# Performance work log

Hardware: AMD Instinct MI355X
Metric: run time of the kernel (lower is better)

## Reference

```python
import jax, jax.numpy as jnp
import numpy as np

B, S, HID = 1, 4096, 2048
H, KVH, D = 8, 4, 256
QR, KR, VR = 6, 2, 2
WINDOW = 1024
SOFTCAP = 50.0
SCALING = 256.0 ** -0.5  # query_pre_attn_scalar ** -0.5
EPS = 1e-6
NEG = -2.3819763e38


def _rope(x, cos, sin):
    # x: [B,S,R,D]; cos/sin: [S,D//2] -> rotate interleaved complex pairs
    xr = x.reshape(*x.shape[:-1], D // 2, 2)
    x1, x2 = xr[..., 0], xr[..., 1]
    c = cos[None, :, None, :]
    s = sin[None, :, None, :]
    out = jnp.stack([x1 * c - x2 * s, x1 * s + x2 * c], axis=-1)
    return out.reshape(x.shape)


def _rmsnorm(x, w):
    var = jnp.mean(x * x, axis=-1, keepdims=True)
    return x * jax.lax.rsqrt(var + EPS) * (1.0 + w)


def setup_inputs() -> dict:
    key = jax.random.key(0)
    ks = jax.random.split(key, 12)
    sc = HID ** -0.5
    pos = np.arange(S, dtype=np.float32)
    inv = 1.0 / (10000.0 ** (np.arange(0, D, 2, dtype=np.float32) / D))
    fr = pos[:, None] * inv[None, :]
    return {
        'hidden_states': jax.random.normal(ks[0], (B, S, HID), jnp.float32),
        'freqs_cos': jnp.asarray(np.cos(fr), jnp.float32),
        'freqs_sin': jnp.asarray(np.sin(fr), jnp.float32),
        'W_A_q': jax.random.normal(ks[1], (H * QR, HID), jnp.float32) * sc,
        'W_A_k': jax.random.normal(ks[2], (KVH * KR, HID), jnp.float32) * sc,
        'W_A_v': jax.random.normal(ks[3], (KVH * VR, HID), jnp.float32) * sc,
        'W_B_q': jax.random.normal(ks[4], (QR * D, HID), jnp.float32) * sc,
        'W_B_k': jax.random.normal(ks[5], (KR * D, HID), jnp.float32) * sc,
        'W_B_v': jax.random.normal(ks[6], (VR * D, HID), jnp.float32) * sc,
        'W_o': jax.random.normal(ks[7], (HID, H * D), jnp.float32) * (H * D) ** -0.5,
        'q_norm_w': jnp.zeros((D,), jnp.float32),
        'k_norm_w': jnp.zeros((D,), jnp.float32),
        'k_cache_A': jnp.zeros((B, S, KVH, KR), jnp.float32),
        'k_cache_B': jnp.zeros((B, S, KR, D), jnp.float32),
        'v_cache_A': jnp.zeros((B, S, KVH, VR), jnp.float32),
        'v_cache_B': jnp.zeros((B, S, VR, D), jnp.float32),
        'kv_write_indices': jnp.arange(S, dtype=jnp.int32),
    }


def reference(hidden_states, freqs_cos, freqs_sin, W_A_q, W_A_k, W_A_v,
              W_B_q, W_B_k, W_B_v, W_o, q_norm_w, k_norm_w,
              k_cache_A, k_cache_B, v_cache_A, v_cache_B, kv_write_indices):
    x = hidden_states  # [B,S,HID]
    # factorized projections
    A_q = (x @ W_A_q.T).reshape(B, S, H, QR)
    A_k = (x @ W_A_k.T).reshape(B, S, KVH, KR)
    A_v = (x @ W_A_v.T).reshape(B, S, KVH, VR)
    B_q = (x @ W_B_q.T).reshape(B, S, QR, D)
    B_k = (x @ W_B_k.T).reshape(B, S, KR, D)
    B_v = (x @ W_B_v.T).reshape(B, S, VR, D)
    # RoPE on head-dim factors of Q and K
    B_q = _rope(B_q, freqs_cos, freqs_sin)
    B_k = _rope(B_k, freqs_cos, freqs_sin)
    # write factors into the TPA KV cache
    k_cache_A = k_cache_A.at[:, kv_write_indices].set(A_k)
    k_cache_B = k_cache_B.at[:, kv_write_indices].set(B_k)
    v_cache_A = v_cache_A.at[:, kv_write_indices].set(A_v)
    v_cache_B = v_cache_B.at[:, kv_write_indices].set(B_v)
    # reconstruct Q/K/V from rank-R tensor products (mean over rank)
    q = jnp.einsum('bshr,bsrd->bshd', A_q, B_q) / QR          # [B,S,H,D]
    k = jnp.einsum('btkr,btrd->btkd', k_cache_A, k_cache_B) / KR  # [B,T,KVH,D]
    v = jnp.einsum('btkr,btrd->btkd', v_cache_A, v_cache_B) / VR
    # QK RMSNorm
    q = _rmsnorm(q, q_norm_w)
    k = _rmsnorm(k, k_norm_w)
    # GQA: expand KV heads to query heads
    rep = H // KVH
    k = jnp.repeat(k, rep, axis=2)  # [B,T,H,D]
    v = jnp.repeat(v, rep, axis=2)
    # scores with softcapping + sliding-window causal mask
    scores = jnp.einsum('bshd,bthd->bhst', q * SCALING, k)
    scores = jnp.tanh(scores / SOFTCAP) * SOFTCAP
    q_pos = kv_write_indices[:, None]        # [S,1]
    k_pos = jnp.arange(S, dtype=jnp.int32)[None, :]  # [1,T]
    diff = q_pos - k_pos
    allowed = (diff >= 0) & (diff < WINDOW)
    scores = jnp.where(allowed[None, None], scores, NEG)
    probs = jax.nn.softmax(scores, axis=-1)
    out = jnp.einsum('bhst,bthd->bshd', probs, v).reshape(B, S, H * D)
    return out @ W_o.T
```

## Files before the change

kernel.cpp:

```cpp
#include <hip/hip_runtime.h>
#include <hip/hip_bf16.h>
#include <cstdint>
#include <cstddef>

constexpr int SEQ   = 4096;
constexpr int HIDN  = 2048;
constexpr int NHEAD = 8;
constexpr int NKVH  = 4;
constexpr int DH    = 256;
constexpr int NPROJ = 2624;
constexpr int NPROJP= 2688;
constexpr int WIN   = 1024;

typedef __attribute__((ext_vector_type(4))) float f32x4;
typedef __attribute__((ext_vector_type(8))) short bf16x8;
typedef unsigned short u16;

__device__ __forceinline__ u16 f2bf(float x) {
  union { float f; uint32_t u; } v; v.f = x;
  uint32_t r = v.u + 0x7fffu + ((v.u >> 16) & 1u);
  return (u16)(r >> 16);
}
__device__ __forceinline__ float bf2f(u16 v) {
  union { uint32_t u; float f; } w; w.u = (uint32_t)v << 16; return w.f;
}

__device__ __forceinline__ uint32_t cvtpk(float lo, float hi) {
  uint32_t r;
  asm("v_cvt_pk_bf16_f32 %0, %1, %2" : "=v"(r) : "v"(lo), "v"(hi));
  return r;
}

__device__ __forceinline__ void gl_lds16(const u16* g, u16* l) {
  __builtin_amdgcn_global_load_lds(
      (const __attribute__((address_space(1))) uint32_t*)g,
      (__attribute__((address_space(3))) uint32_t*)l, 16, 0, 0);
}

__device__ __forceinline__ void sync_vm() {
  asm volatile("s_waitcnt vmcnt(0)" ::: "memory");
  __builtin_amdgcn_s_barrier();
  __builtin_amdgcn_sched_barrier(0);
}

__device__ __forceinline__ int xcd_swz(int wg, int nwg) {
  const int q = nwg >> 3, r = nwg & 7;
  const int xcd = wg & 7, lo = wg >> 3;
  return (xcd < r ? xcd * (q + 1) : r * (q + 1) + (xcd - r) * q) + lo;
}

__global__ __launch_bounds__(256) void k_cvt(const float* __restrict__ src,
                                             u16* __restrict__ dst, int n4) {
  int i = blockIdx.x * 256 + threadIdx.x;
  if (i >= n4) return;
  float4 v = ((const float4*)src)[i];
  ushort4 o; o.x = f2bf(v.x); o.y = f2bf(v.y); o.z = f2bf(v.z); o.w = f2bf(v.w);
  ((ushort4*)dst)[i] = o;
}

__global__ __launch_bounds__(256) void k_wcat(
    const float* __restrict__ waq, const float* __restrict__ wak,
    const float* __restrict__ wav, const float* __restrict__ wbq,
    const float* __restrict__ wbk, const float* __restrict__ wbv,
    u16* __restrict__ wcat) {
  const int r = blockIdx.x;
  const int col0 = threadIdx.x * 8;
  u16* out = wcat + (size_t)r * HIDN + col0;
  const float* src = nullptr; int rr = 0;
  if      (r < 48)   { src = waq; rr = r; }
  else if (r < 56)   { src = wak; rr = r - 48; }
  else if (r < 64)   { src = wav; rr = r - 56; }
  else if (r < 1600) { src = wbq; rr = r - 64; }
  else if (r < 2112) { src = wbk; rr = r - 1600; }
  else if (r < 2624) { src = wbv; rr = r - 2112; }
  if (!src) {
    ushort4 z = {0,0,0,0}; ((ushort4*)out)[0] = z; ((ushort4*)out)[1] = z; return;
  }
  const float* s = src + (size_t)rr * HIDN + col0;
#pragma unroll
  for (int i = 0; i < 2; ++i) {
    float4 v = ((const float4*)s)[i];
    ushort4 o; o.x = f2bf(v.x); o.y = f2bf(v.y); o.z = f2bf(v.z); o.w = f2bf(v.w);
    ((ushort4*)out)[i] = o;
  }
}

template<int OBF16>
__global__ __launch_bounds__(256)
void k_gemm_bt(const u16* __restrict__ A, const u16* __restrict__ Bm,
               void* __restrict__ Cv, int M, int N, int K) {
  __shared__ u16 lA[2][128 * 32];
  __shared__ u16 lB[2][128 * 32];
  const int tid = threadIdx.x;
  const int wid = tid >> 6, lane = tid & 63;
  const int l15 = lane & 15, g = lane >> 4;
  const int nwg = gridDim.x * gridDim.y;
  int wg = xcd_swz(blockIdx.y * gridDim.x + blockIdx.x, nwg);
  const int m0 = (wg / gridDim.x) * 128, n0 = (wg % gridDim.x) * 128;
  const int wr = wid >> 1, wc = wid & 1;
  f32x4 acc[4][4];
#pragma unroll
  for (int m = 0; m < 4; ++m)
#pragma unroll
    for (int n = 0; n < 4; ++n) acc[m][n] = (f32x4){0.f,0.f,0.f,0.f};
  const int NT = K >> 5;

  auto stage = [&](int buf, int kt) {
    const int k0 = kt << 5;
#pragma unroll
    for (int i = 0; i < 2; ++i) {
      const int u = i * 256 + tid;
      const int row = u >> 2, cs = u & 3;
      const int cc = cs ^ ((row >> 1) & 3);
      gl_lds16(A  + (size_t)(m0 + row) * K + k0 + cc * 8, &lA[buf][(i*256 + wid*64) * 8]);
      gl_lds16(Bm + (size_t)(n0 + row) * K + k0 + cc * 8, &lB[buf][(i*256 + wid*64) * 8]);
    }
  };

  stage(0, 0);
  int cur = 0;
  for (int kt = 0; kt < NT; ++kt) {
    __syncthreads();
    if (kt + 1 < NT) stage(cur ^ 1, kt + 1);
    bf16x8 af[4], bfr[4];
#pragma unroll
    for (int m = 0; m < 4; ++m) {
      const int row = wr*64 + m*16 + l15;
      const int cc = g ^ ((row >> 1) & 3);
      af[m] = *(const bf16x8*)&lA[cur][row*32 + cc*8];
    }
#pragma unroll
    for (int n = 0; n < 4; ++n) {
      const int row = wc*64 + n*16 + l15;
      const int cc = g ^ ((row >> 1) & 3);
      bfr[n] = *(const bf16x8*)&lB[cur][row*32 + cc*8];
    }
    __builtin_amdgcn_s_setprio(1);
#pragma unroll
    for (int m = 0; m < 4; ++m)
#pragma unroll
      for (int n = 0; n < 4; ++n)
        acc[m][n] = __builtin_amdgcn_mfma_f32_16x16x32_bf16(af[m], bfr[n], acc[m][n], 0, 0, 0);
    __builtin_amdgcn_s_setprio(0);
    cur ^= 1;
  }
#pragma unroll
  for (int m = 0; m < 4; ++m)
#pragma unroll
    for (int n = 0; n < 4; ++n)
#pragma unroll
      for (int j = 0; j < 4; ++j) {
        const int row = m0 + wr*64 + m*16 + g*4 + j;
        const int col = n0 + wc*64 + n*16 + l15;
        if constexpr (OBF16) ((u16*)Cv)[(size_t)row * N + col] = f2bf(acc[m][n][j]);
        else                 ((float*)Cv)[(size_t)row * N + col] = acc[m][n][j];
      }
}

__global__ __launch_bounds__(256)
void k_qkv(const u16* __restrict__ Y, const float* __restrict__ cosT,
           const float* __restrict__ sinT, const float* __restrict__ qw,
           const float* __restrict__ kw, u16* __restrict__ q_s,
           u16* __restrict__ k_s, u16* __restrict__ v_s) {
  const int s = blockIdx.x;
  const int d = threadIdx.x;
  __shared__ float row[NPROJ];
  __shared__ float red[12][4];
  const u16* yr = Y + (size_t)s * NPROJP;
  for (int u4 = d; u4 < NPROJ/4; u4 += 256) {
    ushort4 v4 = ((const ushort4*)yr)[u4];
    row[u4*4+0] = bf2f(v4.x); row[u4*4+1] = bf2f(v4.y);
    row[u4*4+2] = bf2f(v4.z); row[u4*4+3] = bf2f(v4.w);
  }
  __syncthreads();
  const int i = d >> 1;
  const float cf = cosT[s * 128 + i];
  const float sf = sinT[s * 128 + i];
  const bool odd = d & 1;
  float bq[6], bk[2], bv[2];
#pragma unroll
  for (int r = 0; r < 6; ++r) {
    float x1 = row[64 + r*256 + 2*i], x2 = row[64 + r*256 + 2*i + 1];
    bq[r] = odd ? (x1*sf + x2*cf) : (x1*cf - x2*sf);
  }
#pragma unroll
  for (int r = 0; r < 2; ++r) {
    float x1 = row[1600 + r*256 + 2*i], x2 = row[1600 + r*256 + 2*i + 1];
    bk[r] = odd ? (x1*sf + x2*cf) : (x1*cf - x2*sf);
    bv[r] = row[2112 + r*256 + d];
  }
  float qv[8], kv[4], vv[4];
#pragma unroll
  for (int h = 0; h < 8; ++h) {
    float a = 0.f;
#pragma unroll
    for (int r = 0; r < 6; ++r) a += row[h*6 + r] * bq[r];
    qv[h] = a * (1.0f / 6.0f);
  }
#pragma unroll
  for (int c = 0; c < 4; ++c) {
    kv[c] = (row[48 + c*2]*bk[0] + row[48 + c*2 + 1]*bk[1]) * 0.5f;
    vv[c] = (row[56 + c*2]*bv[0] + row[56 + c*2 + 1]*bv[1]) * 0.5f;
  }
  const int lane = d & 63, wv = d >> 6;
#pragma unroll
  for (int t = 0; t < 12; ++t) {
    float x = (t < 8) ? qv[t] : kv[t - 8];
    float ss = x * x;
#pragma unroll
    for (int off = 32; off > 0; off >>= 1) ss += __shfl_xor(ss, off);
    if (lane == 0) red[t][wv] = ss;
  }
  __syncthreads();
  const float qwf = 1.0f + qw[d], kwf = 1.0f + kw[d];
#pragma unroll
  for (int h = 0; h < 8; ++h) {
    float v = red[h][0] + red[h][1] + red[h][2] + red[h][3];
    float r = rsqrtf(v * (1.0f/256.0f) + 1e-6f);
    q_s[((size_t)s*8 + h)*256 + d] = f2bf(qv[h] * r * qwf * 0.0625f);
  }
#pragma unroll
  for (int c = 0; c < 4; ++c) {
    float v = red[8+c][0] + red[8+c][1] + red[8+c][2] + red[8+c][3];
    float r = rsqrtf(v * (1.0f/256.0f) + 1e-6f);
    k_s[((size_t)s*4 + c)*256 + d] = f2bf(kv[c] * r * kwf);
    v_s[((size_t)s*4 + c)*256 + d] = f2bf(vv[c]);
  }
}

__global__ __launch_bounds__(256)
void k_vt(const u16* __restrict__ v_s, u16* __restrict__ vT) {
  __shared__ u16 tile[64][72];
  const int s0 = blockIdx.x * 64, d0 = blockIdx.y * 64, c = blockIdx.z;
  const int tid = threadIdx.x;
#pragma unroll
  for (int it = 0; it < 2; ++it) {
    const int u = it * 256 + tid;
    const int r = u >> 3, cc = u & 7;
    const u16* s = &v_s[(((size_t)(s0 + r))*4 + c)*256 + d0 + cc*8];
    ushort4 a = *(const ushort4*)s, b = *(const ushort4*)(s + 4);
    tile[r][cc*8+0]=a.x; tile[r][cc*8+1]=a.y; tile[r][cc*8+2]=a.z; tile[r][cc*8+3]=a.w;
    tile[r][cc*8+4]=b.x; tile[r][cc*8+5]=b.y; tile[r][cc*8+6]=b.z; tile[r][cc*8+7]=b.w;
  }
  __syncthreads();
#pragma unroll
  for (int it = 0; it < 2; ++it) {
    const int u = it * 256 + tid;
    const int dr = u >> 3, sc = u & 7;
    ushort4 a, b;
    a.x = tile[sc*8+0][dr]; a.y = tile[sc*8+1][dr]; a.z = tile[sc*8+2][dr]; a.w = tile[sc*8+3][dr];
    b.x = tile[sc*8+4][dr]; b.y = tile[sc*8+5][dr]; b.z = tile[sc*8+6][dr]; b.w = tile[sc*8+7][dr];
    u16* o = vT + ((size_t)c*256 + d0 + dr)*SEQ + s0 + sc*8;
    *(ushort4*)o = a; *(ushort4*)(o + 4) = b;
  }
}

__global__ __launch_bounds__(512, 2)
void k_attn(const u16* __restrict__ q_s, const u16* __restrict__ k_s,
            const u16* __restrict__ vT, const int* __restrict__ idx,
            u16* __restrict__ ao) {
  __shared__ u16 Kt[2][64 * 256];
  __shared__ u16 Vt[2][256 * 64];
  __shared__ u16 Pb[8][16 * 68];
  const int b = blockIdx.x;
  const int c = b & 3, qt = b >> 2;
  const int q0 = qt * 64;
  const int tid = threadIdx.x;
  const int wid = tid >> 6, lane = tid & 63;
  const int l15 = lane & 15, g = lane >> 4;
  const int h = 2*c + (wid >> 2);
  const int qsub = wid & 3;
  const int qrow = q0 + qsub*16 + l15;
  const int qpos = idx[qrow];

  bf16x8 qf[8];
  const u16* qb = q_s + ((size_t)qrow * 8 + h) * 256;
#pragma unroll
  for (int kk = 0; kk < 8; ++kk) qf[kk] = *(const bf16x8*)(qb + kk*32 + g*8);

  const int sw = l15 & 7;
  int kbase[8];
#pragma unroll
  for (int kk = 0; kk < 8; ++kk)
    kbase[kk] = l15*256 + ((((kk<<2)+g) ^ sw) << 3);
  u16* KtF = &Kt[0][0];
  u16* VtF = &Vt[0][0];
  u16* Pw  = &Pb[wid][0];

  f32x4 accO[16];
#pragma unroll
  for (int n = 0; n < 16; ++n) accO[n] = (f32x4){0.f,0.f,0.f,0.f};
  float mrun = -50.0f, lrun = 0.0f;

  int t0 = q0 - (WIN - 1); if (t0 < 0) t0 = 0;
  const int kt_lo = t0 >> 6, kt_hi = qt;

  const u16* kgp = k_s + (size_t)(kt_lo*64 + (tid>>5)) * 1024 + c*256
                   + (((tid & 31) ^ ((tid >> 5) & 7)) << 3);
  const u16* vgp = vT + (size_t)c*1048576 + (size_t)(tid>>3)*4096 + kt_lo*64
                   + (((tid & 7) ^ ((tid >> 3) & 7)) << 3);

  auto stage = [&](int buf) {
#pragma unroll
    for (int i = 0; i < 4; ++i)
      gl_lds16(kgp + i*16384,  &Kt[buf][(i*512 + wid*64) * 8]);
#pragma unroll
    for (int i = 0; i < 4; ++i)
      gl_lds16(vgp + i*262144, &Vt[buf][(i*512 + wid*64) * 8]);
  };

  stage(0);
  int cur = 0;
  for (int kt = kt_lo; kt <= kt_hi; ++kt) {
    const int k0 = kt << 6;
    sync_vm();
    if (kt < kt_hi) { kgp += 65536; vgp += 64; stage(cur ^ 1); }

    const int kco = cur * 16384;
    f32x4 sc[4];
#pragma unroll
    for (int nk = 0; nk < 4; ++nk) sc[nk] = (f32x4){0.f,0.f,0.f,0.f};
    __builtin_amdgcn_s_setprio(1);
#pragma unroll
    for (int nk = 0; nk < 4; ++nk)
#pragma unroll
      for (int kk = 0; kk < 8; ++kk) {
        bf16x8 kf = *(const bf16x8*)&KtF[kco + nk*4096 + kbase[kk]];
        sc[nk] = __builtin_amdgcn_mfma_f32_16x16x32_bf16(kf, qf[kk], sc[nk], 0, 0, 0);
      }
    __builtin_amdgcn_s_setprio(0);

    float tv[16];
#pragma unroll
    for (int nk = 0; nk < 4; ++nk)
#pragma unroll
      for (int j = 0; j < 4; ++j) {
        float u = __builtin_amdgcn_exp2f(sc[nk][j] * 0.05770780163555854f);
        tv[nk*4+j] = fmaf(-100.0f, __builtin_amdgcn_rcpf(1.0f + u), 50.0f);
      }
    if (kt == kt_hi) {
#pragma unroll
      for (int nk = 0; nk < 4; ++nk)
#pragma unroll
        for (int j = 0; j < 4; ++j)
          if (k0 + nk*16 + g*4 + j > qpos) tv[nk*4+j] = -1e38f;
    } else if (kt == kt_lo) {
#pragma unroll
      for (int nk = 0; nk < 4; ++nk)
#pragma unroll
        for (int j = 0; j < 4; ++j)
          if (qpos - (k0 + nk*16 + g*4 + j) > 1023) tv[nk*4+j] = -1e38f;
    }

    float tmax = tv[0];
#pragma unroll
    for (int t = 1; t < 16; ++t) tmax = fmaxf(tmax, tv[t]);
    if (__any(tmax > mrun + 8.0f)) {
      float tq = fmaxf(tmax, __shfl_xor(tmax, 16));
      tq = fmaxf(tq, __shfl_xor(tq, 32));
      const float mnew = fmaxf(mrun, tq);
      const float scale = __builtin_amdgcn_exp2f((mrun - mnew) * 1.442695041f);
      float scj[4];
#pragma unroll
      for (int j = 0; j < 4; ++j) scj[j] = __shfl(scale, g*4 + j);
#pragma unroll
      for (int n = 0; n < 16; ++n) {
        accO[n][0] *= scj[0]; accO[n][1] *= scj[1];
        accO[n][2] *= scj[2]; accO[n][3] *= scj[3];
      }
      lrun *= scale;
      mrun = mnew;
    }
    const float mr2 = mrun * 1.442695041f;
    float p[16];
#pragma unroll
    for (int t = 0; t < 16; ++t) {
      p[t] = __builtin_amdgcn_exp2f(fmaf(tv[t], 1.442695041f, -mr2));
      lrun += p[t];
    }

#pragma unroll
    for (int nk = 0; nk < 4; ++nk) {
      uint2 w = { cvtpk(p[nk*4+0], p[nk*4+1]), cvtpk(p[nk*4+2], p[nk*4+3]) };
      *(uint2*)&Pw[l15*68 + nk*16 + g*4] = w;
    }
    const int vco = cur * 16384;
    __builtin_amdgcn_s_setprio(1);
#pragma unroll
    for (int half = 0; half < 2; ++half) {
      bf16x8 pa = *(const bf16x8*)&Pw[l15*68 + half*32 + g*8];
#pragma unroll
      for (int n = 0; n < 16; ++n) {
        bf16x8 vf = *(const bf16x8*)&VtF[vco + (n*16 + l15)*64
                                         + ((((half<<2)+g) ^ sw) << 3)];
        accO[n] = __builtin_amdgcn_mfma_f32_16x16x32_bf16(pa, vf, accO[n], 0, 0, 0);
      }
    }
    __builtin_amdgcn_s_setprio(0);
    cur ^= 1;
  }

  lrun += __shfl_xor(lrun, 16);
  lrun += __shfl_xor(lrun, 32);
  const float linv = __builtin_amdgcn_rcpf(lrun);
  float lj[4];
#pragma unroll
  for (int j = 0; j < 4; ++j) lj[j] = __shfl(linv, g*4 + j);
#pragma unroll
  for (int n = 0; n < 16; ++n)
#pragma unroll
    for (int j = 0; j < 4; ++j) {
      const int r = q0 + qsub*16 + g*4 + j;
      ao[(size_t)r * HIDN + h*256 + n*16 + l15] = f2bf(accO[n][j] * lj[j]);
    }
}

extern "C" void kernel_launch(void* const* d_in, const int* in_sizes, int n_in,
                              void* d_out, int out_size, void* d_ws, size_t ws_size,
                              hipStream_t stream) {
  const float* x    = (const float*)d_in[0];
  const float* fcos = (const float*)d_in[1];
  const float* fsin = (const float*)d_in[2];
  const float* waq  = (const float*)d_in[3];
  const float* wak  = (const float*)d_in[4];
  const float* wav  = (const float*)d_in[5];
  const float* wbq  = (const float*)d_in[6];
  const float* wbk  = (const float*)d_in[7];
  const float* wbv  = (const float*)d_in[8];
  const float* wo   = (const float*)d_in[9];
  const float* qnw  = (const float*)d_in[10];
  const float* knw  = (const float*)d_in[11];
  const int*   idx  = (const int*)d_in[16];
  float* out = (float*)d_out;

  char* p = (char*)d_ws;
  u16*  xb   = (u16*)p;                 p += (size_t)SEQ*HIDN*2;
  u16*  wcat = (u16*)p;                 p += (size_t)NPROJP*HIDN*2;
  u16*  wob  = (u16*)p;                 p += (size_t)HIDN*HIDN*2;
  u16*  ypr  = (u16*)p;                 p += (size_t)SEQ*NPROJP*2;
  u16*  q_s  = (u16*)p;                 p += (size_t)SEQ*NHEAD*DH*2;
  u16*  k_s  = (u16*)p;                 p += (size_t)SEQ*NKVH*DH*2;
  u16*  v_s  = (u16*)p;                 p += (size_t)SEQ*NKVH*DH*2;
  u16*  vT   = (u16*)p;                 p += (size_t)SEQ*NKVH*DH*2;
  u16*  ao   = (u16*)p;                 p += (size_t)SEQ*HIDN*2;

  k_cvt <<<(SEQ*HIDN/4 + 255)/256, 256, 0, stream>>>(x, xb, SEQ*HIDN/4);
  k_cvt <<<(HIDN*HIDN/4 + 255)/256, 256, 0, stream>>>(wo, wob, HIDN*HIDN/4);
  k_wcat<<<NPROJP, 256, 0, stream>>>(waq, wak, wav, wbq, wbk, wbv, wcat);
  k_gemm_bt<1><<<dim3(NPROJP/128, SEQ/128), 256, 0, stream>>>(xb, wcat, ypr, SEQ, NPROJP, HIDN);
  k_qkv <<<SEQ, 256, 0, stream>>>(ypr, fcos, fsin, qnw, knw, q_s, k_s, v_s);
  k_vt  <<<dim3(SEQ/64, DH/64, NKVH), 256, 0, stream>>>(v_s, vT);
  k_attn<<<dim3(SEQ/64 * NKVH), 512, 0, stream>>>(q_s, k_s, vT, idx, ao);
  k_gemm_bt<0><<<dim3(HIDN/128, SEQ/128), 256, 0, stream>>>(ao, wob, out, SEQ, HIDN, HIDN);
}
```

Baseline: 217.9 us.

## Split key tile across warp pairs with 32-row query blocks and LDS merge

```diff
diff --git a/kernel.cpp b/kernel.cpp
--- a/kernel.cpp
+++ b/kernel.cpp
@@ -261,36 +261,46 @@
             u16* __restrict__ ao) {
   __shared__ u16 Kt[2][64 * 256];
   __shared__ u16 Vt[2][256 * 64];
-  __shared__ u16 Pb[8][16 * 68];
+  __shared__ u16 Pb[8][32 * 40];
+  __shared__ float mlS[4][32][2];
   const int b = blockIdx.x;
   const int c = b & 3, qt = b >> 2;
   const int q0 = qt * 64;
   const int tid = threadIdx.x;
   const int wid = tid >> 6, lane = tid & 63;
   const int l15 = lane & 15, g = lane >> 4;
-  const int h = 2*c + (wid >> 2);
-  const int qsub = wid & 3;
-  const int qrow = q0 + qsub*16 + l15;
-  const int qpos = idx[qrow];
-
-  bf16x8 qf[8];
-  const u16* qb = q_s + ((size_t)qrow * 8 + h) * 256;
-#pragma unroll
-  for (int kk = 0; kk < 8; ++kk) qf[kk] = *(const bf16x8*)(qb + kk*32 + g*8);
-
-  const int sw = l15 & 7;
+  const int kg = wid & 1;
+  const int hh = (wid >> 1) & 1, qp = wid >> 2;
+  const int h = 2*c + hh;
+  const int rg = qp*2 + hh;
+  const int qmin = q0 + qp*32;
+  const int qrowA = qmin + l15, qrowB = qrowA + 16;
+  const int qposA = idx[qrowA], qposB = idx[qrowB];
+
+  bf16x8 qfA[8], qfB[8];
+  { const u16* qa = q_s + ((size_t)qrowA * 8 + h) * 256;
+    const u16* qb = q_s + ((size_t)qrowB * 8 + h) * 256;
+#pragma unroll
+    for (int kk = 0; kk < 8; ++kk) {
+      qfA[kk] = *(const bf16x8*)(qa + kk*32 + g*8);
+      qfB[kk] = *(const bf16x8*)(qb + kk*32 + g*8);
+    } }
+
   int kbase[8];
 #pragma unroll
   for (int kk = 0; kk < 8; ++kk)
-    kbase[kk] = l15*256 + ((((kk<<2)+g) ^ sw) << 3);
+    kbase[kk] = l15*256 + ((((kk<<2)+g) ^ (l15 & 7)) << 3);
   u16* KtF = &Kt[0][0];
   u16* VtF = &Vt[0][0];
   u16* Pw  = &Pb[wid][0];
 
-  f32x4 accO[16];
-#pragma unroll
-  for (int n = 0; n < 16; ++n) accO[n] = (f32x4){0.f,0.f,0.f,0.f};
-  float mrun = -50.0f, lrun = 0.0f;
+  f32x4 accA[16], accB[16];
+#pragma unroll
+  for (int n = 0; n < 16; ++n) {
+    accA[n] = (f32x4){0.f,0.f,0.f,0.f};
+    accB[n] = (f32x4){0.f,0.f,0.f,0.f};
+  }
+  float mA = -50.0f, mB = -50.0f, lA = 0.0f, lB = 0.0f;
 
   int t0 = q0 - (WIN - 1); if (t0 < 0) t0 = 0;
   const int kt_lo = t0 >> 6, kt_hi = qt;
@@ -316,103 +326,156 @@
     sync_vm();
     if (kt < kt_hi) { kgp += 65536; vgp += 64; stage(cur ^ 1); }
 
-    const int kco = cur * 16384;
-    f32x4 sc[4];
-#pragma unroll
-    for (int nk = 0; nk < 4; ++nk) sc[nk] = (f32x4){0.f,0.f,0.f,0.f};
-    __builtin_amdgcn_s_setprio(1);
-#pragma unroll
-    for (int nk = 0; nk < 4; ++nk)
+    const int kh0 = k0 + kg*32;
+    if (kh0 <= qmin + 31 && kh0 + 31 >= qmin - (WIN - 1)) {
+      const int kco = cur*16384 + kg*8192;
+      f32x4 sA0 = (f32x4){0.f,0.f,0.f,0.f}, sA1 = sA0, sB0 = sA0, sB1 = sA0;
+      __builtin_amdgcn_s_setprio(1);
 #pragma unroll
       for (int kk = 0; kk < 8; ++kk) {
-        bf16x8 kf = *(const bf16x8*)&KtF[kco + nk*4096 + kbase[kk]];
-        sc[nk] = __builtin_amdgcn_mfma_f32_16x16x32_bf16(kf, qf[kk], sc[nk], 0, 0, 0);
+        bf16x8 kf0 = *(const bf16x8*)&KtF[kco + kbase[kk]];
+        bf16x8 kf1 = *(const bf16x8*)&KtF[kco + 4096 + kbase[kk]];
+        sA0 = __builtin_amdgcn_mfma_f32_16x16x32_bf16(kf0, qfA[kk], sA0, 0, 0, 0);
+        sB0 = __builtin_amdgcn_mfma_f32_16x16x32_bf16(kf0, qfB[kk], sB0, 0, 0, 0);
+        sA1 = __builtin_amdgcn_mfma_f32_16x16x32_bf16(kf1, qfA[kk], sA1, 0, 0, 0);
+        sB1 = __builtin_amdgcn_mfma_f32_16x16x32_bf16(kf1, qfB[kk], sB1, 0, 0, 0);
       }
-    __builtin_amdgcn_s_setprio(0);
-
-    float tv[16];
-#pragma unroll
-    for (int nk = 0; nk < 4; ++nk)
-#pragma unroll
-      for (int j = 0; j < 4; ++j) {
-        float u = __builtin_amdgcn_exp2f(sc[nk][j] * 0.05770780163555854f);
-        tv[nk*4+j] = fmaf(-100.0f, __builtin_amdgcn_rcpf(1.0f + u), 50.0f);
+      __builtin_amdgcn_s_setprio(0);
+
+      float tvA[8], tvB[8];
+#pragma unroll
+      for (int nk = 0; nk < 2; ++nk)
+#pragma unroll
+        for (int j = 0; j < 4; ++j) {
+          float xa = (nk == 0) ? sA0[j] : sA1[j];
+          float xb = (nk == 0) ? sB0[j] : sB1[j];
+          float ua = __builtin_amdgcn_exp2f(xa * 0.05770780163555854f);
+          float ub = __builtin_amdgcn_exp2f(xb * 0.05770780163555854f);
+          tvA[nk*4+j] = fmaf(-100.0f, __builtin_amdgcn_rcpf(1.0f + ua), 50.0f);
+          tvB[nk*4+j] = fmaf(-100.0f, __builtin_amdgcn_rcpf(1.0f + ub), 50.0f);
+        }
+      if (kt == kt_hi) {
+#pragma unroll
+        for (int nk = 0; nk < 2; ++nk)
+#pragma unroll
+          for (int j = 0; j < 4; ++j) {
+            const int key = kh0 + nk*16 + g*4 + j;
+            if (key > qposA) tvA[nk*4+j] = -1e38f;
+            if (key > qposB) tvB[nk*4+j] = -1e38f;
+          }
+      } else if (kt == kt_lo) {
+#pragma unroll
+        for (int nk = 0; nk < 2; ++nk)
+#pragma unroll
+          for (int j = 0; j < 4; ++j) {
+            const int key = kh0 + nk*16 + g*4 + j;
+            if (qposA - key > WIN - 1) tvA[nk*4+j] = -1e38f;
+            if (qposB - key > WIN - 1) tvB[nk*4+j] = -1e38f;
+          }
       }
-    if (kt == kt_hi) {
-#pragma unroll
-      for (int nk = 0; nk < 4; ++nk)
-#pragma unroll
-        for (int j = 0; j < 4; ++j)
-          if (k0 + nk*16 + g*4 + j > qpos) tv[nk*4+j] = -1e38f;
-    } else if (kt == kt_lo) {
-#pragma unroll
-      for (int nk = 0; nk < 4; ++nk)
-#pragma unroll
-        for (int j = 0; j < 4; ++j)
-          if (qpos - (k0 + nk*16 + g*4 + j) > 1023) tv[nk*4+j] = -1e38f;
-    }
-
-    float tmax = tv[0];
-#pragma unroll
-    for (int t = 1; t < 16; ++t) tmax = fmaxf(tmax, tv[t]);
-    if (__any(tmax > mrun + 8.0f)) {
-      float tq = fmaxf(tmax, __shfl_xor(tmax, 16));
-      tq = fmaxf(tq, __shfl_xor(tq, 32));
-      const float mnew = fmaxf(mrun, tq);
-      const float scale = __builtin_amdgcn_exp2f((mrun - mnew) * 1.442695041f);
-      float scj[4];
-#pragma unroll
-      for (int j = 0; j < 4; ++j) scj[j] = __shfl(scale, g*4 + j);
+
+      float txA = tvA[0], txB = tvB[0];
+#pragma unroll
+      for (int t = 1; t < 8; ++t) { txA = fmaxf(txA, tvA[t]); txB = fmaxf(txB, tvB[t]); }
+      if (__any(fmaxf(txA - mA, txB - mB) > 8.0f)) {
+        float tqA = fmaxf(txA, __shfl_xor(txA, 16));
+        tqA = fmaxf(tqA, __shfl_xor(tqA, 32));
+        float tqB = fmaxf(txB, __shfl_xor(txB, 16));
+        tqB = fmaxf(tqB, __shfl_xor(tqB, 32));
+        const float mnA = fmaxf(mA, tqA), mnB = fmaxf(mB, tqB);
+        const float scA = __builtin_amdgcn_exp2f((mA - mnA) * 1.442695041f);
+        const float scB = __builtin_amdgcn_exp2f((mB - mnB) * 1.442695041f);
+#pragma unroll
+        for (int n = 0; n < 16; ++n) { accA[n] *= scA; accB[n] *= scB; }
+        lA *= scA; lB *= scB; mA = mnA; mB = mnB;
+      }
+      const float cA = mA * 1.442695041f, cB = mB * 1.442695041f;
+      float pA[8], pB[8];
+#pragma unroll
+      for (int t = 0; t < 8; ++t) {
+        pA[t] = __builtin_amdgcn_exp2f(fmaf(tvA[t], 1.442695041f, -cA));
+        pB[t] = __builtin_amdgcn_exp2f(fmaf(tvB[t], 1.442695041f, -cB));
+        lA += pA[t]; lB += pB[t];
+      }
+
+      { uint2 w0 = { cvtpk(pA[0], pA[1]), cvtpk(pA[2], pA[3]) };
+        uint2 w1 = { cvtpk(pA[4], pA[5]), cvtpk(pA[6], pA[7]) };
+        *(uint2*)&Pw[l15*40 + g*4]       = w0;
+        *(uint2*)&Pw[l15*40 + 16 + g*4]  = w1;
+        uint2 x0 = { cvtpk(pB[0], pB[1]), cvtpk(pB[2], pB[3]) };
+        uint2 x1 = { cvtpk(pB[4], pB[5]), cvtpk(pB[6], pB[7]) };
+        *(uint2*)&Pw[(16+l15)*40 + g*4]      = x0;
+        *(uint2*)&Pw[(16+l15)*40 + 16 + g*4] = x1; }
+      bf16x8 paA = *(const bf16x8*)&Pw[l15*40 + g*8];
+      bf16x8 paB = *(const bf16x8*)&Pw[(16+l15)*40 + g*8];
+
+      const int vco = cur * 16384;
+      __builtin_amdgcn_s_setprio(1);
 #pragma unroll
       for (int n = 0; n < 16; ++n) {
-        accO[n][0] *= scj[0]; accO[n][1] *= scj[1];
-        accO[n][2] *= scj[2]; accO[n][3] *= scj[3];
+        const int dr = n*16 + l15;
+        bf16x8 vf = *(const bf16x8*)&VtF[vco + dr*64 + ((((kg<<2)+g) ^ (dr & 7)) << 3)];
+        accA[n] = __builtin_amdgcn_mfma_f32_16x16x32_bf16(vf, paA, accA[n], 0, 0, 0);
+        accB[n] = __builtin_amdgcn_mfma_f32_16x16x32_bf16(vf, paB, accB[n], 0, 0, 0);
       }
-      lrun *= scale;
-      mrun = mnew;
-    }
-    const float mr2 = mrun * 1.442695041f;
-    float p[16];
-#pragma unroll
-    for (int t = 0; t < 16; ++t) {
-      p[t] = __builtin_amdgcn_exp2f(fmaf(tv[t], 1.442695041f, -mr2));
-      lrun += p[t];
-    }
-
-#pragma unroll
-    for (int nk = 0; nk < 4; ++nk) {
-      uint2 w = { cvtpk(p[nk*4+0], p[nk*4+1]), cvtpk(p[nk*4+2], p[nk*4+3]) };
-      *(uint2*)&Pw[l15*68 + nk*16 + g*4] = w;
-    }
-    const int vco = cur * 16384;
-    __builtin_amdgcn_s_setprio(1);
-#pragma unroll
-    for (int half = 0; half < 2; ++half) {
-      bf16x8 pa = *(const bf16x8*)&Pw[l15*68 + half*32 + g*8];
-#pragma unroll
-      for (int n = 0; n < 16; ++n) {
-        bf16x8 vf = *(const bf16x8*)&VtF[vco + (n*16 + l15)*64
-                                         + ((((half<<2)+g) ^ sw) << 3)];
-        accO[n] = __builtin_amdgcn_mfma_f32_16x16x32_bf16(pa, vf, accO[n], 0, 0, 0);
-      }
-    }
-    __builtin_amdgcn_s_setprio(0);
+      __builtin_amdgcn_s_setprio(0);
+    }
     cur ^= 1;
   }
 
-  lrun += __shfl_xor(lrun, 16);
-  lrun += __shfl_xor(lrun, 32);
-  const float linv = __builtin_amdgcn_rcpf(lrun);
-  float lj[4];
-#pragma unroll
-  for (int j = 0; j < 4; ++j) lj[j] = __shfl(linv, g*4 + j);
-#pragma unroll
-  for (int n = 0; n < 16; ++n)
-#pragma unroll
-    for (int j = 0; j < 4; ++j) {
-      const int r = q0 + qsub*16 + g*4 + j;
-      ao[(size_t)r * HIDN + h*256 + n*16 + l15] = f2bf(accO[n][j] * lj[j]);
-    }
+  lA += __shfl_xor(lA, 16); lA += __shfl_xor(lA, 32);
+  lB += __shfl_xor(lB, 16); lB += __shfl_xor(lB, 32);
+
+  float* scr = (rg < 2 ? (float*)&Kt[0][0] : (float*)&Vt[0][0]) + (size_t)(rg & 1) * 8192;
+  __syncthreads();
+  if (kg == 0) {
+#pragma unroll
+    for (int n = 0; n < 16; ++n) {
+      const int p0 = (((n<<3) + (g<<1))    ) ^ (l15 & 7);
+      const int p1 = (((n<<3) + (g<<1)) + 1) ^ (l15 & 7);
+      ((float2*)scr)[l15*128 + p0]      = make_float2(accA[n][0], accA[n][1]);
+      ((float2*)scr)[l15*128 + p1]      = make_float2(accA[n][2], accA[n][3]);
+      ((float2*)scr)[(16+l15)*128 + p0] = make_float2(accB[n][0], accB[n][1]);
+      ((float2*)scr)[(16+l15)*128 + p1] = make_float2(accB[n][2], accB[n][3]);
+    }
+    if (g == 0) {
+      mlS[rg][l15][0] = mA;      mlS[rg][l15][1] = lA;
+      mlS[rg][16+l15][0] = mB;   mlS[rg][16+l15][1] = lB;
+    }
+    __syncthreads();
+  } else {
+    __syncthreads();
+    const float pmA = mlS[rg][l15][0],    plA = mlS[rg][l15][1];
+    const float pmB = mlS[rg][16+l15][0], plB = mlS[rg][16+l15][1];
+    const float MA = fmaxf(pmA, mA), MB = fmaxf(pmB, mB);
+    const float aw0 = __builtin_amdgcn_exp2f((pmA - MA) * 1.442695041f);
+    const float aw1 = __builtin_amdgcn_exp2f((mA  - MA) * 1.442695041f);
+    const float bw0 = __builtin_amdgcn_exp2f((pmB - MB) * 1.442695041f);
+    const float bw1 = __builtin_amdgcn_exp2f((mB  - MB) * 1.442695041f);
+    const float ari = __builtin_amdgcn_rcpf(aw0*plA + aw1*lA);
+    const float bri = __builtin_amdgcn_rcpf(bw0*plB + bw1*lB);
+#pragma unroll
+    for (int n = 0; n < 16; ++n) {
+      const int p0 = (((n<<3) + (g<<1))    ) ^ (l15 & 7);
+      const int p1 = (((n<<3) + (g<<1)) + 1) ^ (l15 & 7);
+      float2 a0 = ((float2*)scr)[l15*128 + p0];
+      float2 a1 = ((float2*)scr)[l15*128 + p1];
+      float2 b0 = ((float2*)scr)[(16+l15)*128 + p0];
+      float2 b1 = ((float2*)scr)[(16+l15)*128 + p1];
+      const float oA0 = (aw0*a0.x + aw1*accA[n][0]) * ari;
+      const float oA1 = (aw0*a0.y + aw1*accA[n][1]) * ari;
+      const float oA2 = (aw0*a1.x + aw1*accA[n][2]) * ari;
+      const float oA3 = (aw0*a1.y + aw1*accA[n][3]) * ari;
+      const float oB0 = (bw0*b0.x + bw1*accB[n][0]) * bri;
+      const float oB1 = (bw0*b0.y + bw1*accB[n][1]) * bri;
+      const float oB2 = (bw0*b1.x + bw1*accB[n][2]) * bri;
+      const float oB3 = (bw0*b1.y + bw1*accB[n][3]) * bri;
+      uint2 wa = { cvtpk(oA0, oA1), cvtpk(oA2, oA3) };
+      uint2 wb = { cvtpk(oB0, oB1), cvtpk(oB2, oB3) };
+      *(uint2*)&ao[(size_t)qrowA * HIDN + h*256 + n*16 + g*4] = wa;
+      *(uint2*)&ao[(size_t)qrowB * HIDN + h*256 + n*16 + g*4] = wb;
+    }
+  }
 }
 
 extern "C" void kernel_launch(void* const* d_in, const int* in_sizes, int n_in,
```

Result: slower. 226.4 us (+3.9%).

## Replace 128x128 GEMM with 256x256 tile, BK=64, phased LDS pipelining

Applied to the files above, without the earlier changes.

```diff
diff --git a/kernel.cpp b/kernel.cpp
--- a/kernel.cpp
+++ b/kernel.cpp
@@ -9,7 +9,7 @@
 constexpr int NKVH  = 4;
 constexpr int DH    = 256;
 constexpr int NPROJ = 2624;
-constexpr int NPROJP= 2688;
+constexpr int NPROJP= 2816;
 constexpr int WIN   = 1024;
 
 typedef __attribute__((ext_vector_type(4))) float f32x4;
@@ -39,6 +39,12 @@
 
 __device__ __forceinline__ void sync_vm() {
   asm volatile("s_waitcnt vmcnt(0)" ::: "memory");
+  __builtin_amdgcn_s_barrier();
+  __builtin_amdgcn_sched_barrier(0);
+}
+
+__device__ __forceinline__ void phase_barrier() {
+  asm volatile("" ::: "memory");
   __builtin_amdgcn_s_barrier();
   __builtin_amdgcn_sched_barrier(0);
 }
@@ -86,71 +92,135 @@
 }
 
 template<int OBF16>
-__global__ __launch_bounds__(256)
-void k_gemm_bt(const u16* __restrict__ A, const u16* __restrict__ Bm,
+__global__ __launch_bounds__(512, 2)
+void k_gemm256(const u16* __restrict__ A, const u16* __restrict__ Bm,
                void* __restrict__ Cv, int M, int N, int K) {
-  __shared__ u16 lA[2][128 * 32];
-  __shared__ u16 lB[2][128 * 32];
+  __shared__ u16 lA[2][256 * 64];
+  __shared__ u16 lB[2][256 * 64];
   const int tid = threadIdx.x;
   const int wid = tid >> 6, lane = tid & 63;
   const int l15 = lane & 15, g = lane >> 4;
+  const int wr = wid >> 2, wc = wid & 3;
   const int nwg = gridDim.x * gridDim.y;
   int wg = xcd_swz(blockIdx.y * gridDim.x + blockIdx.x, nwg);
-  const int m0 = (wg / gridDim.x) * 128, n0 = (wg % gridDim.x) * 128;
-  const int wr = wid >> 1, wc = wid & 1;
-  f32x4 acc[4][4];
-#pragma unroll
-  for (int m = 0; m < 4; ++m)
+  const int m0 = (wg / gridDim.x) * 256, n0 = (wg % gridDim.x) * 256;
+
+  f32x4 acc[8][4];
+#pragma unroll
+  for (int m = 0; m < 8; ++m)
 #pragma unroll
     for (int n = 0; n < 4; ++n) acc[m][n] = (f32x4){0.f,0.f,0.f,0.f};
-  const int NT = K >> 5;
-
-  auto stage = [&](int buf, int kt) {
-    const int k0 = kt << 5;
-#pragma unroll
-    for (int i = 0; i < 2; ++i) {
-      const int u = i * 256 + tid;
-      const int row = u >> 2, cs = u & 3;
-      const int cc = cs ^ ((row >> 1) & 3);
-      gl_lds16(A  + (size_t)(m0 + row) * K + k0 + cc * 8, &lA[buf][(i*256 + wid*64) * 8]);
-      gl_lds16(Bm + (size_t)(n0 + row) * K + k0 + cc * 8, &lB[buf][(i*256 + wid*64) * 8]);
-    }
+  const int NT = K >> 6;
+
+  const int srow = tid >> 3;
+  const int scc  = (tid & 7) ^ (srow & 7);
+  const u16* ag = A  + (size_t)(m0 + srow) * K + scc * 8;
+  const u16* bg = Bm + (size_t)(n0 + srow) * K + scc * 8;
+
+  auto stB = [&](int buf, int kt) {
+    const size_t ko = (size_t)kt << 6;
+#pragma unroll
+    for (int j = 0; j < 4; ++j)
+      gl_lds16(bg + (size_t)(j*64) * K + ko, &lB[buf][j*4096 + wid*512]);
   };
-
-  stage(0, 0);
-  int cur = 0;
-  for (int kt = 0; kt < NT; ++kt) {
-    __syncthreads();
-    if (kt + 1 < NT) stage(cur ^ 1, kt + 1);
-    bf16x8 af[4], bfr[4];
-#pragma unroll
-    for (int m = 0; m < 4; ++m) {
-      const int row = wr*64 + m*16 + l15;
-      const int cc = g ^ ((row >> 1) & 3);
-      af[m] = *(const bf16x8*)&lA[cur][row*32 + cc*8];
-    }
-#pragma unroll
-    for (int n = 0; n < 4; ++n) {
-      const int row = wc*64 + n*16 + l15;
-      const int cc = g ^ ((row >> 1) & 3);
-      bfr[n] = *(const bf16x8*)&lB[cur][row*32 + cc*8];
-    }
+  auto stA0 = [&](int buf, int kt) {
+    const size_t ko = (size_t)kt << 6;
+    gl_lds16(ag + ko,                   &lA[buf][wid*512]);
+    gl_lds16(ag + (size_t)64 * K + ko,  &lA[buf][4096 + wid*512]);
+  };
+  auto stA1 = [&](int buf, int kt) {
+    const size_t ko = (size_t)kt << 6;
+    gl_lds16(ag + (size_t)128 * K + ko, &lA[buf][8192  + wid*512]);
+    gl_lds16(ag + (size_t)192 * K + ko, &lA[buf][12288 + wid*512]);
+  };
+
+  const int sw8 = l15 & 7;
+  int aoff[2], boff[2];
+#pragma unroll
+  for (int kk = 0; kk < 2; ++kk) {
+    aoff[kk] = (wr*128 + l15)*64 + (((kk*4 + g) ^ sw8) << 3);
+    boff[kk] = (wc*64  + l15)*64 + (((kk*4 + g) ^ sw8) << 3);
+  }
+  const u16* lAf = &lA[0][0];
+  const u16* lBf = &lB[0][0];
+
+  stB(0, 0); stA0(0, 0); stA1(0, 0);
+
+  for (int t = 0; t < NT; ++t) {
+    const int buf = t & 1, nb = buf ^ 1;
+    const int ab = buf * 16384, bb = buf * 16384;
+    const bool more = (t + 1 < NT);
+    bf16x8 af[8], f0, f1;
+
+    if (more) {
+      stB(nb, t + 1);
+      asm volatile("s_waitcnt vmcnt(4)" ::: "memory");
+    } else {
+      asm volatile("s_waitcnt vmcnt(0)" ::: "memory");
+    }
+    __builtin_amdgcn_s_barrier();
+    __builtin_amdgcn_sched_barrier(0);
+#pragma unroll
+    for (int m = 0; m < 8; ++m) af[m] = *(const bf16x8*)&lAf[ab + aoff[0] + m*1024];
+    f0 = *(const bf16x8*)&lBf[bb + boff[0]];
+    f1 = *(const bf16x8*)&lBf[bb + boff[0] + 1024];
     __builtin_amdgcn_s_setprio(1);
 #pragma unroll
-    for (int m = 0; m < 4; ++m)
-#pragma unroll
-      for (int n = 0; n < 4; ++n)
-        acc[m][n] = __builtin_amdgcn_mfma_f32_16x16x32_bf16(af[m], bfr[n], acc[m][n], 0, 0, 0);
+    for (int m = 0; m < 8; ++m) {
+      acc[m][0] = __builtin_amdgcn_mfma_f32_16x16x32_bf16(af[m], f0, acc[m][0], 0, 0, 0);
+      acc[m][1] = __builtin_amdgcn_mfma_f32_16x16x32_bf16(af[m], f1, acc[m][1], 0, 0, 0);
+    }
     __builtin_amdgcn_s_setprio(0);
-    cur ^= 1;
-  }
-#pragma unroll
-  for (int m = 0; m < 4; ++m)
+    phase_barrier();
+
+    f0 = *(const bf16x8*)&lBf[bb + boff[0] + 2048];
+    f1 = *(const bf16x8*)&lBf[bb + boff[0] + 3072];
+    if (more) stA0(nb, t + 1);
+    phase_barrier();
+    __builtin_amdgcn_s_setprio(1);
+#pragma unroll
+    for (int m = 0; m < 8; ++m) {
+      acc[m][2] = __builtin_amdgcn_mfma_f32_16x16x32_bf16(af[m], f0, acc[m][2], 0, 0, 0);
+      acc[m][3] = __builtin_amdgcn_mfma_f32_16x16x32_bf16(af[m], f1, acc[m][3], 0, 0, 0);
+    }
+    __builtin_amdgcn_s_setprio(0);
+    phase_barrier();
+
+#pragma unroll
+    for (int m = 0; m < 8; ++m) af[m] = *(const bf16x8*)&lAf[ab + aoff[1] + m*1024];
+    f0 = *(const bf16x8*)&lBf[bb + boff[1]];
+    f1 = *(const bf16x8*)&lBf[bb + boff[1] + 1024];
+    if (more) stA1(nb, t + 1);
+    phase_barrier();
+    __builtin_amdgcn_s_setprio(1);
+#pragma unroll
+    for (int m = 0; m < 8; ++m) {
+      acc[m][0] = __builtin_amdgcn_mfma_f32_16x16x32_bf16(af[m], f0, acc[m][0], 0, 0, 0);
+      acc[m][1] = __builtin_amdgcn_mfma_f32_16x16x32_bf16(af[m], f1, acc[m][1], 0, 0, 0);
+    }
+    __builtin_amdgcn_s_setprio(0);
+    phase_barrier();
+
+    f0 = *(const bf16x8*)&lBf[bb + boff[1] + 2048];
+    f1 = *(const bf16x8*)&lBf[bb + boff[1] + 3072];
+    phase_barrier();
+    __builtin_amdgcn_s_setprio(1);
+#pragma unroll
+    for (int m = 0; m < 8; ++m) {
+      acc[m][2] = __builtin_amdgcn_mfma_f32_16x16x32_bf16(af[m], f0, acc[m][2], 0, 0, 0);
+      acc[m][3] = __builtin_amdgcn_mfma_f32_16x16x32_bf16(af[m], f1, acc[m][3], 0, 0, 0);
+    }
+    __builtin_amdgcn_s_setprio(0);
+    phase_barrier();
+  }
+
+#pragma unroll
+  for (int m = 0; m < 8; ++m)
 #pragma unroll
     for (int n = 0; n < 4; ++n)
 #pragma unroll
       for (int j = 0; j < 4; ++j) {
-        const int row = m0 + wr*64 + m*16 + g*4 + j;
+        const int row = m0 + wr*128 + m*16 + g*4 + j;
         const int col = n0 + wc*64 + n*16 + l15;
         if constexpr (OBF16) ((u16*)Cv)[(size_t)row * N + col] = f2bf(acc[m][n][j]);
         else                 ((float*)Cv)[(size_t)row * N + col] = acc[m][n][j];
@@ -447,9 +517,9 @@
   k_cvt <<<(SEQ*HIDN/4 + 255)/256, 256, 0, stream>>>(x, xb, SEQ*HIDN/4);
   k_cvt <<<(HIDN*HIDN/4 + 255)/256, 256, 0, stream>>>(wo, wob, HIDN*HIDN/4);
   k_wcat<<<NPROJP, 256, 0, stream>>>(waq, wak, wav, wbq, wbk, wbv, wcat);
-  k_gemm_bt<1><<<dim3(NPROJP/128, SEQ/128), 256, 0, stream>>>(xb, wcat, ypr, SEQ, NPROJP, HIDN);
+  k_gemm256<1><<<dim3(NPROJP/256, SEQ/256), 512, 0, stream>>>(xb, wcat, ypr, SEQ, NPROJP, HIDN);
   k_qkv <<<SEQ, 256, 0, stream>>>(ypr, fcos, fsin, qnw, knw, q_s, k_s, v_s);
   k_vt  <<<dim3(SEQ/64, DH/64, NKVH), 256, 0, stream>>>(v_s, vT);
   k_attn<<<dim3(SEQ/64 * NKVH), 512, 0, stream>>>(q_s, k_s, vT, idx, ao);
-  k_gemm_bt<0><<<dim3(HIDN/128, SEQ/128), 256, 0, stream>>>(ao, wob, out, SEQ, HIDN, HIDN);
-}
+  k_gemm256<0><<<dim3(HIDN/256, SEQ/256), 512, 0, stream>>>(ao, wob, out, SEQ, HIDN, HIDN);
+}
```

After: 253.6 us. 16.4% more time.

## Split attention KV range across two blocks and merge partial softmax results

Applied to the files above, without the earlier changes.

```diff
diff --git a/kernel.cpp b/kernel.cpp
--- a/kernel.cpp
+++ b/kernel.cpp
@@ -14,6 +14,7 @@
 
 typedef __attribute__((ext_vector_type(4))) float f32x4;
 typedef __attribute__((ext_vector_type(8))) short bf16x8;
+typedef __attribute__((ext_vector_type(4))) short bf16x4;
 typedef unsigned short u16;
 
 __device__ __forceinline__ u16 f2bf(float x) {
@@ -39,6 +40,13 @@
 
 __device__ __forceinline__ void sync_vm() {
   asm volatile("s_waitcnt vmcnt(0)" ::: "memory");
+  __builtin_amdgcn_s_barrier();
+  __builtin_amdgcn_sched_barrier(0);
+}
+
+__device__ __forceinline__ void sync_lgkm() {
+  asm volatile("s_waitcnt lgkmcnt(0)" ::: "memory");
+  __builtin_amdgcn_sched_barrier(0);
   __builtin_amdgcn_s_barrier();
   __builtin_amdgcn_sched_barrier(0);
 }
@@ -255,15 +263,14 @@
   }
 }
 
-__global__ __launch_bounds__(512, 2)
+__global__ __launch_bounds__(512, 4)
 void k_attn(const u16* __restrict__ q_s, const u16* __restrict__ k_s,
             const u16* __restrict__ vT, const int* __restrict__ idx,
-            u16* __restrict__ ao) {
-  __shared__ u16 Kt[2][64 * 256];
-  __shared__ u16 Vt[2][256 * 64];
-  __shared__ u16 Pb[8][16 * 68];
+            u16* __restrict__ op, float2* __restrict__ ml) {
+  __shared__ u16 Kt[64 * 256];
+  __shared__ u16 Vt[256 * 64];
   const int b = blockIdx.x;
-  const int c = b & 3, qt = b >> 2;
+  const int c = b & 3, qt = (b >> 2) & 63, sp = b >> 8;
   const int q0 = qt * 64;
   const int tid = threadIdx.x;
   const int wid = tid >> 6, lane = tid & 63;
@@ -283,9 +290,6 @@
 #pragma unroll
   for (int kk = 0; kk < 8; ++kk)
     kbase[kk] = l15*256 + ((((kk<<2)+g) ^ sw) << 3);
-  u16* KtF = &Kt[0][0];
-  u16* VtF = &Vt[0][0];
-  u16* Pw  = &Pb[wid][0];
 
   f32x4 accO[16];
 #pragma unroll
@@ -294,29 +298,27 @@
 
   int t0 = q0 - (WIN - 1); if (t0 < 0) t0 = 0;
   const int kt_lo = t0 >> 6, kt_hi = qt;
-
-  const u16* kgp = k_s + (size_t)(kt_lo*64 + (tid>>5)) * 1024 + c*256
+  const int kt0 = kt_lo + sp;
+
+  const u16* kgp = k_s + (size_t)(kt0*64 + (tid>>5)) * 1024 + c*256
                    + (((tid & 31) ^ ((tid >> 5) & 7)) << 3);
-  const u16* vgp = vT + (size_t)c*1048576 + (size_t)(tid>>3)*4096 + kt_lo*64
+  const u16* vgp = vT + (size_t)c*1048576 + (size_t)(tid>>3)*4096 + kt0*64
                    + (((tid & 7) ^ ((tid >> 3) & 7)) << 3);
 
-  auto stage = [&](int buf) {
+  auto stage = [&]() {
 #pragma unroll
     for (int i = 0; i < 4; ++i)
-      gl_lds16(kgp + i*16384,  &Kt[buf][(i*512 + wid*64) * 8]);
+      gl_lds16(kgp + i*16384,  &Kt[(i*512 + wid*64) * 8]);
 #pragma unroll
     for (int i = 0; i < 4; ++i)
-      gl_lds16(vgp + i*262144, &Vt[buf][(i*512 + wid*64) * 8]);
+      gl_lds16(vgp + i*262144, &Vt[(i*512 + wid*64) * 8]);
   };
 
-  stage(0);
-  int cur = 0;
-  for (int kt = kt_lo; kt <= kt_hi; ++kt) {
+  if (kt0 <= kt_hi) stage();
+  for (int kt = kt0; kt <= kt_hi; kt += 2) {
     const int k0 = kt << 6;
     sync_vm();
-    if (kt < kt_hi) { kgp += 65536; vgp += 64; stage(cur ^ 1); }
-
-    const int kco = cur * 16384;
+
     f32x4 sc[4];
 #pragma unroll
     for (int nk = 0; nk < 4; ++nk) sc[nk] = (f32x4){0.f,0.f,0.f,0.f};
@@ -325,7 +327,7 @@
     for (int nk = 0; nk < 4; ++nk)
 #pragma unroll
       for (int kk = 0; kk < 8; ++kk) {
-        bf16x8 kf = *(const bf16x8*)&KtF[kco + nk*4096 + kbase[kk]];
+        bf16x8 kf = *(const bf16x8*)&Kt[nk*4096 + kbase[kk]];
         sc[nk] = __builtin_amdgcn_mfma_f32_16x16x32_bf16(kf, qf[kk], sc[nk], 0, 0, 0);
       }
     __builtin_amdgcn_s_setprio(0);
@@ -379,40 +381,63 @@
       lrun += p[t];
     }
 
+    __builtin_amdgcn_s_setprio(1);
 #pragma unroll
     for (int nk = 0; nk < 4; ++nk) {
-      uint2 w = { cvtpk(p[nk*4+0], p[nk*4+1]), cvtpk(p[nk*4+2], p[nk*4+3]) };
-      *(uint2*)&Pw[l15*68 + nk*16 + g*4] = w;
-    }
-    const int vco = cur * 16384;
-    __builtin_amdgcn_s_setprio(1);
-#pragma unroll
-    for (int half = 0; half < 2; ++half) {
-      bf16x8 pa = *(const bf16x8*)&Pw[l15*68 + half*32 + g*8];
+      union { uint32_t u[2]; bf16x4 v; } pu;
+      pu.u[0] = cvtpk(p[nk*4+0], p[nk*4+1]);
+      pu.u[1] = cvtpk(p[nk*4+2], p[nk*4+3]);
 #pragma unroll
       for (int n = 0; n < 16; ++n) {
-        bf16x8 vf = *(const bf16x8*)&VtF[vco + (n*16 + l15)*64
-                                         + ((((half<<2)+g) ^ sw) << 3)];
-        accO[n] = __builtin_amdgcn_mfma_f32_16x16x32_bf16(pa, vf, accO[n], 0, 0, 0);
+        const int dr = n*16 + l15;
+        bf16x4 vf = *(const bf16x4*)&Vt[dr*64 + (((2*nk + (g>>1)) ^ sw) << 3) + (g&1)*4];
+        accO[n] = __builtin_amdgcn_mfma_f32_16x16x16bf16_1k(pu.v, vf, accO[n], 0, 0, 0);
       }
     }
     __builtin_amdgcn_s_setprio(0);
-    cur ^= 1;
+
+    sync_lgkm();
+    if (kt + 2 <= kt_hi) { kgp += 131072; vgp += 128; stage(); }
   }
 
   lrun += __shfl_xor(lrun, 16);
   lrun += __shfl_xor(lrun, 32);
-  const float linv = __builtin_amdgcn_rcpf(lrun);
-  float lj[4];
-#pragma unroll
-  for (int j = 0; j < 4; ++j) lj[j] = __shfl(linv, g*4 + j);
+  if (g == 0) ml[(size_t)sp*SEQ*NHEAD + (size_t)qrow*NHEAD + h] = make_float2(mrun, lrun);
+  u16* opS = op + (size_t)sp*SEQ*HIDN;
 #pragma unroll
   for (int n = 0; n < 16; ++n)
 #pragma unroll
     for (int j = 0; j < 4; ++j) {
       const int r = q0 + qsub*16 + g*4 + j;
-      ao[(size_t)r * HIDN + h*256 + n*16 + l15] = f2bf(accO[n][j] * lj[j]);
-    }
+      opS[(size_t)r * HIDN + h*256 + n*16 + l15] = f2bf(accO[n][j]);
+    }
+}
+
+__global__ __launch_bounds__(256)
+void k_mrg(const u16* __restrict__ op, const float2* __restrict__ ml,
+           u16* __restrict__ ao) {
+  const int q = blockIdx.x;
+  const int h = threadIdx.x >> 5;
+  const int dd = (threadIdx.x & 31) * 8;
+  const float2 a = ml[(size_t)q*NHEAD + h];
+  const float2 b = ml[(size_t)SEQ*NHEAD + (size_t)q*NHEAD + h];
+  const float M = fmaxf(a.x, b.x);
+  float w0 = __builtin_amdgcn_exp2f((a.x - M) * 1.442695041f);
+  float w1 = __builtin_amdgcn_exp2f((b.x - M) * 1.442695041f);
+  const float r = __builtin_amdgcn_rcpf(w0 * a.y + w1 * b.y);
+  w0 *= r; w1 *= r;
+  const size_t base = (size_t)q * HIDN + h*256 + dd;
+  bf16x8 o0 = *(const bf16x8*)&op[base];
+  bf16x8 o1 = *(const bf16x8*)&op[(size_t)SEQ*HIDN + base];
+  ushort4 lo, hi;
+  u16 ov[8];
+#pragma unroll
+  for (int j = 0; j < 8; ++j)
+    ov[j] = f2bf(w0 * bf2f((u16)o0[j]) + w1 * bf2f((u16)o1[j]));
+  lo.x = ov[0]; lo.y = ov[1]; lo.z = ov[2]; lo.w = ov[3];
+  hi.x = ov[4]; hi.y = ov[5]; hi.z = ov[6]; hi.w = ov[7];
+  *(ushort4*)&ao[base] = lo;
+  *(ushort4*)&ao[base + 4] = hi;
 }
 
 extern "C" void kernel_launch(void* const* d_in, const int* in_sizes, int n_in,
@@ -443,6 +468,8 @@
   u16*  v_s  = (u16*)p;                 p += (size_t)SEQ*NKVH*DH*2;
   u16*  vT   = (u16*)p;                 p += (size_t)SEQ*NKVH*DH*2;
   u16*  ao   = (u16*)p;                 p += (size_t)SEQ*HIDN*2;
+  u16*  op   = (u16*)p;                 p += (size_t)2*SEQ*HIDN*2;
+  float2* ml = (float2*)p;              p += (size_t)2*SEQ*NHEAD*sizeof(float2);
 
   k_cvt <<<(SEQ*HIDN/4 + 255)/256, 256, 0, stream>>>(x, xb, SEQ*HIDN/4);
   k_cvt <<<(HIDN*HIDN/4 + 255)/256, 256, 0, stream>>>(wo, wob, HIDN*HIDN/4);
@@ -450,6 +477,7 @@
   k_gemm_bt<1><<<dim3(NPROJP/128, SEQ/128), 256, 0, stream>>>(xb, wcat, ypr, SEQ, NPROJP, HIDN);
   k_qkv <<<SEQ, 256, 0, stream>>>(ypr, fcos, fsin, qnw, knw, q_s, k_s, v_s);
   k_vt  <<<dim3(SEQ/64, DH/64, NKVH), 256, 0, stream>>>(v_s, vT);
-  k_attn<<<dim3(SEQ/64 * NKVH), 512, 0, stream>>>(q_s, k_s, vT, idx, ao);
+  k_attn<<<dim3(2 * SEQ/64 * NKVH), 512, 0, stream>>>(q_s, k_s, vT, idx, op, ml);
+  k_mrg <<<SEQ, 256, 0, stream>>>(op, ml, ao);
   k_gemm_bt<0><<<dim3(HIDN/128, SEQ/128), 256, 0, stream>>>(ao, wob, out, SEQ, HIDN, HIDN);
 }
```

Measured after the change: 300.7 us. 38.0% more time.
